# Optimization experiments

Measured on AMD Instinct MI355X. Metric: run time of the kernel, lower is better.

Reference implementation:

```python
import jax, jax.numpy as jnp
import numpy as np


def conv2d_same(x, w, b=None):
    # x: [B,C,H,W], w: [O,I,kh,kw], stride 1, SAME padding (pad=1 for 3x3)
    out = jax.lax.conv_general_dilated(
        x, w, window_strides=(1, 1), padding='SAME',
        dimension_numbers=('NCHW', 'OIHW', 'NCHW'))
    if b is not None:
        out = out + b[None, :, None, None]
    return out


def deform_conv(x, offset, wd, k=3, pad=1, dg=4):
    # DCNv1: per-location offset-guided bilinear sampling + weighted accumulation.
    # x: [B,C,H,W]; offset: [B, dg*k*k*2, H, W] as (dy,dx) pairs per kernel tap;
    # wd: [O, C, k, k] (bias-free, as in mmcv DeformConv).
    B, C, H, W = x.shape
    cg = C // dg          # channels per deformable group
    K = k * k
    off = offset.reshape(B, dg, K, 2, H, W)
    dy, dx = off[:, :, :, 0], off[:, :, :, 1]          # [B,dg,K,H,W]
    ky = (jnp.arange(K) // k - pad).astype(x.dtype)    # kernel row offsets
    kx = (jnp.arange(K) % k - pad).astype(x.dtype)     # kernel col offsets
    hh = jnp.arange(H, dtype=x.dtype)
    ww = jnp.arange(W, dtype=x.dtype)
    py = dy + ky[None, None, :, None, None] + hh[None, None, None, :, None]
    px = dx + kx[None, None, :, None, None] + ww[None, None, None, None, :]
    y0 = jnp.floor(py); x0 = jnp.floor(px)
    wy1 = py - y0; wy0 = 1.0 - wy1
    wx1 = px - x0; wx0 = 1.0 - wx1
    xg = x.reshape(B, dg, cg, H * W)

    def gather(yi, xi):
        # zero outside the feature map (implicit zero padding of bilinear kernel)
        valid = (yi >= 0) & (yi < H) & (xi >= 0) & (xi < W)
        yc = jnp.clip(yi, 0, H - 1).astype(jnp.int32)
        xc = jnp.clip(xi, 0, W - 1).astype(jnp.int32)
        idx = (yc * W + xc).reshape(B, dg, 1, K * H * W)
        g = jnp.take_along_axis(xg, jnp.broadcast_to(idx, (B, dg, cg, K * H * W)), axis=-1)
        g = g.reshape(B, dg, cg, K, H, W)
        return g * valid[:, :, None].astype(x.dtype)

    val = (gather(y0, x0) * (wy0 * wx0)[:, :, None]
           + gather(y0, x0 + 1) * (wy0 * wx1)[:, :, None]
           + gather(y0 + 1, x0) * (wy1 * wx0)[:, :, None]
           + gather(y0 + 1, x0 + 1) * (wy1 * wx1)[:, :, None])  # [B,dg,cg,K,H,W]
    wr = wd.reshape(wd.shape[0], dg, cg, K)
    return jnp.einsum('ogck,bgckhw->bohw', wr, val)


def setup_inputs() -> dict:
    key = jax.random.key(0)
    k1, k2, k3, k4 = jax.random.split(key, 4)
    B, C, H, W = 8, 256, 64, 64
    dg, ks = 4, 3
    x = jax.random.normal(k1, (B, C, H, W), dtype=jnp.float32)
    w1 = jax.random.normal(k2, (C, C, 3, 3), dtype=jnp.float32) * 0.01
    b1 = jnp.zeros((C,), dtype=jnp.float32)
    w2 = jax.random.normal(k3, (dg * ks * ks * 2, C, 3, 3), dtype=jnp.float32) * 0.01
    b2 = jnp.zeros((dg * ks * ks * 2,), dtype=jnp.float32)
    wd = jax.random.normal(k4, (C, C, ks, ks), dtype=jnp.float32) * 0.01
    return {'x': x, 'w1': w1, 'b1': b1, 'w2': w2, 'b2': b2, 'wd': wd}


def reference(x, w1, b1, w2, b2, wd):
    # offset branch uses x.detach() in the original
    xd = jax.lax.stop_gradient(x)
    offset = conv2d_same(conv2d_same(xd, w1, b1), w2, b2)
    return jax.nn.relu(deform_conv(x, offset, wd, k=3, pad=1, dg=4))
```

## Files before the change

### kernel.cpp

```cpp
#include <hip/hip_runtime.h>
#include <hip/hip_bf16.h>


typedef __attribute__((ext_vector_type(8))) short bf16x8;
typedef __attribute__((ext_vector_type(4))) float f32x4;

static __device__ __forceinline__ ushort f2bf(float f) {
  __hip_bfloat16 h = __float2bfloat16(f);
  return *reinterpret_cast<ushort*>(&h);
}
static __device__ __forceinline__ float bf2f(ushort u) {
  union { uint u32; float f; } cv;
  cv.u32 = ((uint)u) << 16;
  return cv.f;
}

__global__ __launch_bounds__(256) void prep_weights(
    const float* __restrict__ w1, const float* __restrict__ w2,
    const float* __restrict__ wd,
    ushort* __restrict__ wt1, ushort* __restrict__ wt2,
    ushort* __restrict__ wtd) {
  const int N1 = 72 * 4 * 256 * 8;
  const int N2 = 72 * 4 * 128 * 8;
  const int N3 = 72 * 4 * 256 * 8;
  int total = N1 + N2 + N3;
  for (int i = blockIdx.x * 256 + threadIdx.x; i < total; i += gridDim.x * 256) {
    if (i < N1) {
      int e = i & 7, co = (i >> 3) & 255, p = (i >> 11) & 3, tk = i >> 13;
      int ti = tk >> 1, half = tk & 1;
      int kk = ti >> 2, ch = ti & 3;
      int cc = half * 32 + p * 8 + e;
      wt1[i] = f2bf(w1[(co * 256 + ch * 64 + cc) * 9 + kk]);
    } else if (i < N1 + N2) {
      int d = i - N1;
      int e = d & 7, co = (d >> 3) & 127, p = (d >> 10) & 3, tk = d >> 12;
      int ti = tk >> 1, half = tk & 1;
      int kk = ti >> 2, ch = ti & 3;
      int cc = half * 32 + p * 8 + e;
      wt2[d] = (co < 72) ? f2bf(w2[(co * 256 + ch * 64 + cc) * 9 + kk])
                         : (ushort)0;
    } else {
      int d = i - N1 - N2;
      int e = d & 7, co = (d >> 3) & 255, p = (d >> 11) & 3, tk = d >> 13;
      int ti = tk >> 1, half = tk & 1;
      int g = ti / 9, kkt = ti - g * 9;
      int c = half * 32 + p * 8 + e;
      wtd[d] = f2bf(wd[(co * 256 + g * 64 + c) * 9 + kkt]);
    }
  }
}

__global__ __launch_bounds__(256) void transpose_x(
    const float* __restrict__ x, ushort* __restrict__ xt) {
  int id = blockIdx.x;
  int y = id & 63, bg = id >> 6;
  int c = threadIdx.x & 63, xi = threadIdx.x >> 6;
  const float* ip = x + (((size_t)bg) << 18) + ((size_t)c << 12) + y * 64;
  ushort* op = xt + (((size_t)bg) << 18) + (size_t)y * 4096 + c;
#pragma unroll
  for (int j = 0; j < 16; ++j) {
    int xx = xi * 16 + j;
    op[(size_t)xx * 64] = f2bf(ip[xx]);
  }
}

template <int MODE, int NFR>
__global__ __launch_bounds__(256, 3) void fa_mfma10(
    const ushort* __restrict__ inT,
    const float* __restrict__ off,
    const ushort* __restrict__ wBs,
    ushort* __restrict__ parA,
    ushort* __restrict__ parB) {
  constexpr int CO_TILE = NFR * 16;
  constexpr int SUB_U = CO_TILE * 32;
  constexpr int NCALLS = (SUB_U * 2) / 4096;
  constexpr int NRN = (MODE == 1) ? 8 : 2;
  __shared__ __align__(16) ushort Blds[2][SUB_U];

  int id = blockIdx.x;
  int id2 = (id & 7) * 128 + (id >> 3);
  int khalf = id2 & 1;
  int rest = id2 >> 1;
  int h = rest & 63, b = rest >> 6;
  int t = threadIdx.x;
  int wv = t >> 6, lane = t & 63;
  int ml = lane & 15, kc = lane >> 4;
  int pcol = wv * 16 + ml;
  ushort* par = khalf ? parB : parA;

  auto stage = [&](int s, int buf) {
    int tk = khalf * 36 + s;
    const char* src0 = (const char*)wBs + (size_t)tk * (SUB_U * 2) + t * 16;
    ushort* dst0 = &Blds[buf][t * 8];
#pragma unroll
    for (int m = 0; m < NCALLS; ++m) {
      __builtin_amdgcn_global_load_lds(
          (const __attribute__((address_space(1))) void*)(src0 + m * 4096),
          (__attribute__((address_space(3))) void*)(dst0 + m * 2048), 16, 0, 0);
    }
  };

  const bf16x8 bz = {0, 0, 0, 0, 0, 0, 0, 0};
  bf16x8 aCur0, aCur1;
  bf16x8 rN[NRN];
  float wsv[4];
  float2 offA;

  auto issueA0 = [&](int tap) {
    int kk = tap >> 2, chunk = tap & 3;
    int ky = kk / 3, kx = kk - ky * 3;
    int gy = h + ky - 1, gx = pcol + kx - 1;
    bool inb = (gy >= 0) & (gy < 64) & (gx >= 0) & (gx < 64);
    const ushort* p =
        inT + ((((size_t)(b * 4 + chunk) << 12) + gy * 64 + gx) << 6) + kc * 8;
    rN[0] = bz;
    rN[1] = bz;
    if (inb) {
      rN[0] = *(const bf16x8*)p;
      rN[1] = *(const bf16x8*)(p + 32);
    }
  };
  auto finishA0 = [&]() {
    aCur0 = rN[0];
    aCur1 = rN[1];
  };

  auto loadOff = [&](int tap) {
    int g = tap / 9, kkt = tap - 9 * (tap / 9);
    int ch = g * 18 + kkt * 2;
    const float* offp = off + (((size_t)b * 72 + ch) << 12) + h * 64 + pcol;
    offA.x = offp[0];
    offA.y = offp[4096];
  };
  auto issueA1 = [&](int tap) {
    int g = tap / 9, kkt = tap - 9 * (tap / 9);
    int ky = kkt / 3, kx = kkt - ky * 3;
    const ushort* base = inT + (((size_t)(b * 4 + g)) << 18) + kc * 8;
    float py = (float)(h + ky - 1) + offA.x;
    float pxf = (float)(pcol + kx - 1) + offA.y;
    float y0f = floorf(py), x0f = floorf(pxf);
    float wy1 = py - y0f, wx1 = pxf - x0f;
    float wy0 = 1.f - wy1, wx0 = 1.f - wx1;
    int y0 = (int)y0f, x0i = (int)x0f;
    int y1 = y0 + 1, x1i = x0i + 1;
    bool vy0 = (y0 >= 0) & (y0 < 64);
    bool vy1 = (y1 >= 0) & (y1 < 64);
    bool vx0 = (x0i >= 0) & (x0i < 64);
    bool vx1 = (x1i >= 0) & (x1i < 64);
    wsv[0] = (vy0 & vx0) ? wy0 * wx0 : 0.f;
    wsv[1] = (vy0 & vx1) ? wy0 * wx1 : 0.f;
    wsv[2] = (vy1 & vx0) ? wy1 * wx0 : 0.f;
    wsv[3] = (vy1 & vx1) ? wy1 * wx1 : 0.f;
    int yc0 = min(max(y0, 0), 63), yc1 = min(max(y1, 0), 63);
    int xc0 = min(max(x0i, 0), 63), xc1 = min(max(x1i, 0), 63);
    const ushort* p00 = base + ((yc0 * 64 + xc0) << 6);
    const ushort* p01 = base + ((yc0 * 64 + xc1) << 6);
    const ushort* p10 = base + ((yc1 * 64 + xc0) << 6);
    const ushort* p11 = base + ((yc1 * 64 + xc1) << 6);
    rN[0] = *(const bf16x8*)p00;
    rN[1] = *(const bf16x8*)(p00 + 32);
    rN[2] = *(const bf16x8*)p01;
    rN[3] = *(const bf16x8*)(p01 + 32);
    rN[4] = *(const bf16x8*)p10;
    rN[5] = *(const bf16x8*)(p10 + 32);
    rN[6] = *(const bf16x8*)p11;
    rN[7] = *(const bf16x8*)(p11 + 32);
  };
  auto finishA1 = [&]() {
    float w00 = wsv[0], w01 = wsv[1], w10 = wsv[2], w11 = wsv[3];
#pragma unroll
    for (int ks = 0; ks < 2; ++ks) {
      bf16x8 q00 = rN[0 + ks], q01 = rN[2 + ks];
      bf16x8 q10 = rN[4 + ks], q11 = rN[6 + ks];
      bf16x8 av;
#pragma unroll
      for (int jj = 0; jj < 8; ++jj) {
        float v = w00 * bf2f((ushort)q00[jj]) + w01 * bf2f((ushort)q01[jj]) +
                  w10 * bf2f((ushort)q10[jj]) + w11 * bf2f((ushort)q11[jj]);
        av[jj] = (short)f2bf(v);
      }
      if (ks == 0) aCur0 = av; else aCur1 = av;
    }
  };

  f32x4 acc[NFR];
#pragma unroll
  for (int j = 0; j < NFR; ++j) acc[j] = (f32x4){0.f, 0.f, 0.f, 0.f};

  auto domfma = [&](bf16x8 a, int buf) {
    __builtin_amdgcn_s_setprio(1);
#pragma unroll
    for (int nf = 0; nf < NFR; ++nf) {
      bf16x8 bq = *(const bf16x8*)&Blds[buf][(kc * CO_TILE + nf * 16 + ml) * 8];
      acc[nf] = __builtin_amdgcn_mfma_f32_16x16x32_bf16(a, bq, acc[nf], 0, 0, 0);
    }
    __builtin_amdgcn_s_setprio(0);
  };

  const int tap0 = khalf * 18;

  if (MODE == 1) {
    loadOff(tap0);
    issueA1(tap0);
    loadOff(tap0 + 1);
    finishA1();
  } else {
    issueA0(tap0);
    finishA0();
  }
  stage(0, 0);
  __syncthreads();

  for (int tp = 0; tp < 18; ++tp) {
    int tap = tap0 + tp;
    if (2 * tp + 1 < 36) stage(2 * tp + 1, 1);
    if (tp < 17) { if (MODE == 1) issueA1(tap + 1); else issueA0(tap + 1); }
    if (MODE == 1 && tp < 16) loadOff(tap + 2);
    domfma(aCur0, 0);
    __syncthreads();
    if (2 * tp + 2 < 36) stage(2 * tp + 2, 0);
    domfma(aCur1, 1);
    if (tp < 17) { if (MODE == 1) finishA1(); else finishA0(); }
    __syncthreads();
  }

  size_t wbase = ((size_t)((b * 64 + h) * 4 + wv)) * (NFR * 4 * 64);
#pragma unroll
  for (int nf = 0; nf < NFR; ++nf)
#pragma unroll
    for (int ri = 0; ri < 4; ++ri)
      par[wbase + (nf * 4 + ri) * 64 + lane] = f2bf(acc[nf][ri]);
}


__global__ __launch_bounds__(256) void reduce_c1(
    const ushort* __restrict__ p0, const ushort* __restrict__ p1,
    const float* __restrict__ bias, ushort* __restrict__ t1) {
  const int N = 8 * 4 * 4096 * 8;
  for (int i = blockIdx.x * 256 + threadIdx.x; i < N; i += gridDim.x * 256) {
    int cg = i & 7;
    int pix = (i >> 3) & 4095;
    int g = (i >> 15) & 3;
    int b = i >> 17;
    int h = pix >> 6, col = pix & 63;
    int wv = col >> 4, rr = col & 15;
    int rq = rr >> 2, ri = rr & 3;
    int cp = g * 64 + cg * 8;
    int nf = cp >> 4, mlb = cp & 15;
    size_t idx = ((size_t)((b * 64 + h) * 4 + wv)) * 4096 +
                 (nf * 4 + ri) * 64 + rq * 16 + mlb;
    bf16x8 a = *(const bf16x8*)(p0 + idx);
    bf16x8 c = *(const bf16x8*)(p1 + idx);
    bf16x8 o;
#pragma unroll
    for (int j = 0; j < 8; ++j)
      o[j] = (short)f2bf(bf2f((ushort)a[j]) + bf2f((ushort)c[j]) + bias[cp + j]);
    *(bf16x8*)(t1 + ((size_t)(b * 4 + g) * 4096 + pix) * 64 + cg * 8) = o;
  }
}

__global__ __launch_bounds__(256) void reduce_c2(
    const ushort* __restrict__ p0, const ushort* __restrict__ p1,
    const float* __restrict__ bias, float* __restrict__ out) {
  const int N = 8 * 72 * 1024;
  for (int i = blockIdx.x * 256 + threadIdx.x; i < N; i += gridDim.x * 256) {
    int p4 = i & 1023;
    int r = i >> 10;
    int co = r % 72, b = r / 72;
    int h = p4 >> 4;
    int col0 = (p4 & 15) * 4;
    int wv = col0 >> 4, rq = (col0 >> 2) & 3;
    int nf = co >> 4, ml = co & 15;
    size_t base = ((size_t)((b * 64 + h) * 4 + wv)) * 2048 +
                  nf * 256 + rq * 16 + ml;
    float bv = bias[co];
    float4 o;
    o.x = bf2f(p0[base +   0]) + bf2f(p1[base +   0]) + bv;
    o.y = bf2f(p0[base +  64]) + bf2f(p1[base +  64]) + bv;
    o.z = bf2f(p0[base + 128]) + bf2f(p1[base + 128]) + bv;
    o.w = bf2f(p0[base + 192]) + bf2f(p1[base + 192]) + bv;
    *(float4*)(out + (((size_t)b * 72 + co) << 12) + p4 * 4) = o;
  }
}

__global__ __launch_bounds__(256) void reduce_df(
    const ushort* __restrict__ p0, const ushort* __restrict__ p1,
    float* __restrict__ out) {
  const int N = 8 * 256 * 1024;
  for (int i = blockIdx.x * 256 + threadIdx.x; i < N; i += gridDim.x * 256) {
    int p4 = i & 1023;
    int co = (i >> 10) & 255;
    int b = i >> 18;
    int h = p4 >> 4;
    int col0 = (p4 & 15) * 4;
    int wv = col0 >> 4, rq = (col0 >> 2) & 3;
    int nf = co >> 4, ml = co & 15;
    size_t base = ((size_t)((b * 64 + h) * 4 + wv)) * 4096 +
                  nf * 256 + rq * 16 + ml;
    float4 o;
    o.x = fmaxf(bf2f(p0[base +   0]) + bf2f(p1[base +   0]), 0.f);
    o.y = fmaxf(bf2f(p0[base +  64]) + bf2f(p1[base +  64]), 0.f);
    o.z = fmaxf(bf2f(p0[base + 128]) + bf2f(p1[base + 128]), 0.f);
    o.w = fmaxf(bf2f(p0[base + 192]) + bf2f(p1[base + 192]), 0.f);
    *(float4*)(out + (((size_t)b * 256 + co) << 12) + p4 * 4) = o;
  }
}

extern "C" void kernel_launch(void* const* d_in, const int* in_sizes, int n_in,
                              void* d_out, int out_size, void* d_ws, size_t ws_size,
                              hipStream_t stream) {
  const float* x  = (const float*)d_in[0];
  const float* w1 = (const float*)d_in[1];
  const float* b1 = (const float*)d_in[2];
  const float* w2 = (const float*)d_in[3];
  const float* b2 = (const float*)d_in[4];
  const float* wd = (const float*)d_in[5];

  char* wsb = (char*)d_ws;
  float*  off_buf = (float*)wsb;
  ushort* xt      = (ushort*)(wsb + 9437184);
  ushort* wt1     = (ushort*)(wsb + 26214400);
  ushort* wt2     = (ushort*)(wsb + 27394048);
  ushort* wtd     = (ushort*)(wsb + 27983872);
  ushort* par0    = (ushort*)(wsb + 29163520);
  ushort* par1    = (ushort*)(wsb + 45940736);

  prep_weights<<<2048, 256, 0, stream>>>(w1, w2, wd, wt1, wt2, wtd);
  transpose_x<<<2048, 256, 0, stream>>>(x, xt);

  ushort* t1 = (ushort*)d_out;

  fa_mfma10<0, 16><<<1024, 256, 0, stream>>>(xt, nullptr, wt1, par0, par1);
  reduce_c1<<<2048, 256, 0, stream>>>(par0, par1, b1, t1);

  fa_mfma10<0, 8><<<1024, 256, 0, stream>>>(t1, nullptr, wt2, par0, par1);
  reduce_c2<<<1024, 256, 0, stream>>>(par0, par1, b2, off_buf);

  fa_mfma10<1, 16><<<1024, 256, 0, stream>>>(xt, off_buf, wtd, par0, par1);
  reduce_df<<<2048, 256, 0, stream>>>(par0, par1, (float*)d_out);
}
```

Before: 236.2 us.

## Drop split-K halves and fuse bias/relu epilogue into MFMA conv kernels

Each conv/deform kernel now runs the full 36-tap reduction in one block instead of splitting it across two blocks that write bf16 partials, and writes the final output with bias or relu directly from the accumulators. The three separate reduce kernels and the partial-sum workspace traffic go away, along with one bf16 rounding of partials. In exchange the grid shrinks from 1024 to 512 blocks, which halves parallelism on a large CU count, and the epilogue now issues scalar, less coalesced stores. Launch bounds also go from 3 to 4 waves per SIMD hint.

```diff
diff --git a/kernel.cpp b/kernel.cpp
--- a/kernel.cpp
+++ b/kernel.cpp
@@ -64,13 +64,14 @@
   }
 }
 
-template <int MODE, int NFR>
-__global__ __launch_bounds__(256, 3) void fa_mfma10(
+template <int MODE, int NFR, int OUTK>
+__global__ __launch_bounds__(256, 4) void fa_mfma11(
     const ushort* __restrict__ inT,
     const float* __restrict__ off,
     const ushort* __restrict__ wBs,
-    ushort* __restrict__ parA,
-    ushort* __restrict__ parB) {
+    const float* __restrict__ bias,
+    void* __restrict__ outp,
+    int co_total, int co_write) {
   constexpr int CO_TILE = NFR * 16;
   constexpr int SUB_U = CO_TILE * 32;
   constexpr int NCALLS = (SUB_U * 2) / 4096;
@@ -78,19 +79,15 @@
   __shared__ __align__(16) ushort Blds[2][SUB_U];
 
   int id = blockIdx.x;
-  int id2 = (id & 7) * 128 + (id >> 3);
-  int khalf = id2 & 1;
-  int rest = id2 >> 1;
-  int h = rest & 63, b = rest >> 6;
+  int id2 = (id & 7) * 64 + (id >> 3);
+  int h = id2 & 63, b = id2 >> 6;
   int t = threadIdx.x;
   int wv = t >> 6, lane = t & 63;
   int ml = lane & 15, kc = lane >> 4;
   int pcol = wv * 16 + ml;
-  ushort* par = khalf ? parB : parA;
-
-  auto stage = [&](int s, int buf) {
-    int tk = khalf * 36 + s;
-    const char* src0 = (const char*)wBs + (size_t)tk * (SUB_U * 2) + t * 16;
+
+  auto stage = [&](int sg, int buf) {
+    const char* src0 = (const char*)wBs + (size_t)sg * (SUB_U * 2) + t * 16;
     ushort* dst0 = &Blds[buf][t * 8];
 #pragma unroll
     for (int m = 0; m < NCALLS; ++m) {
@@ -197,112 +194,52 @@
     __builtin_amdgcn_s_setprio(0);
   };
 
-  const int tap0 = khalf * 18;
-
   if (MODE == 1) {
-    loadOff(tap0);
-    issueA1(tap0);
-    loadOff(tap0 + 1);
+    loadOff(0);
+    issueA1(0);
+    loadOff(1);
     finishA1();
   } else {
-    issueA0(tap0);
+    issueA0(0);
     finishA0();
   }
   stage(0, 0);
   __syncthreads();
 
-  for (int tp = 0; tp < 18; ++tp) {
-    int tap = tap0 + tp;
-    if (2 * tp + 1 < 36) stage(2 * tp + 1, 1);
-    if (tp < 17) { if (MODE == 1) issueA1(tap + 1); else issueA0(tap + 1); }
-    if (MODE == 1 && tp < 16) loadOff(tap + 2);
+  for (int tp = 0; tp < 36; ++tp) {
+    if (2 * tp + 1 < 72) stage(2 * tp + 1, 1);
+    if (tp < 35) { if (MODE == 1) issueA1(tp + 1); else issueA0(tp + 1); }
+    if (MODE == 1 && tp < 34) loadOff(tp + 2);
     domfma(aCur0, 0);
     __syncthreads();
-    if (2 * tp + 2 < 36) stage(2 * tp + 2, 0);
+    if (2 * tp + 2 < 72) stage(2 * tp + 2, 0);
     domfma(aCur1, 1);
-    if (tp < 17) { if (MODE == 1) finishA1(); else finishA0(); }
+    if (tp < 35) { if (MODE == 1) finishA1(); else finishA0(); }
     __syncthreads();
   }
 
-  size_t wbase = ((size_t)((b * 64 + h) * 4 + wv)) * (NFR * 4 * 64);
-#pragma unroll
-  for (int nf = 0; nf < NFR; ++nf)
-#pragma unroll
-    for (int ri = 0; ri < 4; ++ri)
-      par[wbase + (nf * 4 + ri) * 64 + lane] = f2bf(acc[nf][ri]);
-}
-
-
-__global__ __launch_bounds__(256) void reduce_c1(
-    const ushort* __restrict__ p0, const ushort* __restrict__ p1,
-    const float* __restrict__ bias, ushort* __restrict__ t1) {
-  const int N = 8 * 4 * 4096 * 8;
-  for (int i = blockIdx.x * 256 + threadIdx.x; i < N; i += gridDim.x * 256) {
-    int cg = i & 7;
-    int pix = (i >> 3) & 4095;
-    int g = (i >> 15) & 3;
-    int b = i >> 17;
-    int h = pix >> 6, col = pix & 63;
-    int wv = col >> 4, rr = col & 15;
-    int rq = rr >> 2, ri = rr & 3;
-    int cp = g * 64 + cg * 8;
-    int nf = cp >> 4, mlb = cp & 15;
-    size_t idx = ((size_t)((b * 64 + h) * 4 + wv)) * 4096 +
-                 (nf * 4 + ri) * 64 + rq * 16 + mlb;
-    bf16x8 a = *(const bf16x8*)(p0 + idx);
-    bf16x8 c = *(const bf16x8*)(p1 + idx);
-    bf16x8 o;
-#pragma unroll
-    for (int j = 0; j < 8; ++j)
-      o[j] = (short)f2bf(bf2f((ushort)a[j]) + bf2f((ushort)c[j]) + bias[cp + j]);
-    *(bf16x8*)(t1 + ((size_t)(b * 4 + g) * 4096 + pix) * 64 + cg * 8) = o;
-  }
-}
-
-__global__ __launch_bounds__(256) void reduce_c2(
-    const ushort* __restrict__ p0, const ushort* __restrict__ p1,
-    const float* __restrict__ bias, float* __restrict__ out) {
-  const int N = 8 * 72 * 1024;
-  for (int i = blockIdx.x * 256 + threadIdx.x; i < N; i += gridDim.x * 256) {
-    int p4 = i & 1023;
-    int r = i >> 10;
-    int co = r % 72, b = r / 72;
-    int h = p4 >> 4;
-    int col0 = (p4 & 15) * 4;
-    int wv = col0 >> 4, rq = (col0 >> 2) & 3;
-    int nf = co >> 4, ml = co & 15;
-    size_t base = ((size_t)((b * 64 + h) * 4 + wv)) * 2048 +
-                  nf * 256 + rq * 16 + ml;
-    float bv = bias[co];
-    float4 o;
-    o.x = bf2f(p0[base +   0]) + bf2f(p1[base +   0]) + bv;
-    o.y = bf2f(p0[base +  64]) + bf2f(p1[base +  64]) + bv;
-    o.z = bf2f(p0[base + 128]) + bf2f(p1[base + 128]) + bv;
-    o.w = bf2f(p0[base + 192]) + bf2f(p1[base + 192]) + bv;
-    *(float4*)(out + (((size_t)b * 72 + co) << 12) + p4 * 4) = o;
-  }
-}
-
-__global__ __launch_bounds__(256) void reduce_df(
-    const ushort* __restrict__ p0, const ushort* __restrict__ p1,
-    float* __restrict__ out) {
-  const int N = 8 * 256 * 1024;
-  for (int i = blockIdx.x * 256 + threadIdx.x; i < N; i += gridDim.x * 256) {
-    int p4 = i & 1023;
-    int co = (i >> 10) & 255;
-    int b = i >> 18;
-    int h = p4 >> 4;
-    int col0 = (p4 & 15) * 4;
-    int wv = col0 >> 4, rq = (col0 >> 2) & 3;
-    int nf = co >> 4, ml = co & 15;
-    size_t base = ((size_t)((b * 64 + h) * 4 + wv)) * 4096 +
-                  nf * 256 + rq * 16 + ml;
-    float4 o;
-    o.x = fmaxf(bf2f(p0[base +   0]) + bf2f(p1[base +   0]), 0.f);
-    o.y = fmaxf(bf2f(p0[base +  64]) + bf2f(p1[base +  64]), 0.f);
-    o.z = fmaxf(bf2f(p0[base + 128]) + bf2f(p1[base + 128]), 0.f);
-    o.w = fmaxf(bf2f(p0[base + 192]) + bf2f(p1[base + 192]), 0.f);
-    *(float4*)(out + (((size_t)b * 256 + co) << 12) + p4 * 4) = o;
+  int rq = lane >> 4;
+#pragma unroll
+  for (int nf = 0; nf < NFR; ++nf) {
+    int cog = nf * 16 + ml;
+    if (cog < co_write) {
+      float bv = (OUTK == 2) ? 0.f : bias[cog];
+#pragma unroll
+      for (int ri = 0; ri < 4; ++ri) {
+        int pxe = wv * 16 + rq * 4 + ri;
+        float v = acc[nf][ri] + bv;
+        if (OUTK == 0) {
+          int g_out = cog >> 6, ci = cog & 63;
+          ((ushort*)outp)[((((size_t)(b * 4 + g_out) << 12) + h * 64 + pxe) << 6) + ci] =
+              f2bf(v);
+        } else if (OUTK == 1) {
+          ((float*)outp)[(((size_t)b * co_total + cog) << 12) + h * 64 + pxe] = v;
+        } else {
+          ((float*)outp)[(((size_t)b * co_total + cog) << 12) + h * 64 + pxe] =
+              fmaxf(v, 0.f);
+        }
+      }
+    }
   }
 }
 
@@ -322,20 +259,18 @@
   ushort* wt1     = (ushort*)(wsb + 26214400);
   ushort* wt2     = (ushort*)(wsb + 27394048);
   ushort* wtd     = (ushort*)(wsb + 27983872);
-  ushort* par0    = (ushort*)(wsb + 29163520);
-  ushort* par1    = (ushort*)(wsb + 45940736);
 
   prep_weights<<<2048, 256, 0, stream>>>(w1, w2, wd, wt1, wt2, wtd);
   transpose_x<<<2048, 256, 0, stream>>>(x, xt);
 
   ushort* t1 = (ushort*)d_out;
 
-  fa_mfma10<0, 16><<<1024, 256, 0, stream>>>(xt, nullptr, wt1, par0, par1);
-  reduce_c1<<<2048, 256, 0, stream>>>(par0, par1, b1, t1);
-
-  fa_mfma10<0, 8><<<1024, 256, 0, stream>>>(t1, nullptr, wt2, par0, par1);
-  reduce_c2<<<1024, 256, 0, stream>>>(par0, par1, b2, off_buf);
-
-  fa_mfma10<1, 16><<<1024, 256, 0, stream>>>(xt, off_buf, wtd, par0, par1);
-  reduce_df<<<2048, 256, 0, stream>>>(par0, par1, (float*)d_out);
-}
+  fa_mfma11<0, 16, 0><<<512, 256, 0, stream>>>(
+      xt, nullptr, wt1, b1, t1, 256, 256);
+
+  fa_mfma11<0, 8, 1><<<512, 256, 0, stream>>>(
+      t1, nullptr, wt2, b2, off_buf, 72, 72);
+
+  fa_mfma11<1, 16, 2><<<512, 256, 0, stream>>>(
+      xt, off_buf, wtd, nullptr, d_out, 256, 256);
+}
```

After: 214.5 us. 1.1x faster.
